# Kernel optimization log

Measured on AMD Instinct MI355X. Metric: run time of the kernel, lower is better.

The kernel has to match this reference:

```python
import jax, jax.numpy as jnp
import numpy as np

IN_CH = 128
INTER = max(IN_CH // 8, 1)  # 16

def setup_inputs() -> dict:
    key = jax.random.key(0)
    ks = jax.random.split(key, 10)
    B, C, D, H, W = 2, IN_CH, 16, 24, 24
    s = 1.0 / np.sqrt(C)
    so = 1.0 / np.sqrt(INTER)
    return {
        "x":  jax.random.normal(ks[0], (B, C, D, H, W), dtype=jnp.float32),
        "Wq": jax.random.normal(ks[1], (INTER, C), dtype=jnp.float32) * s,
        "bq": jax.random.normal(ks[2], (INTER,), dtype=jnp.float32) * 0.01,
        "Wk": jax.random.normal(ks[3], (INTER, C), dtype=jnp.float32) * s,
        "bk": jax.random.normal(ks[4], (INTER,), dtype=jnp.float32) * 0.01,
        "Wv": jax.random.normal(ks[5], (INTER, C), dtype=jnp.float32) * s,
        "bv": jax.random.normal(ks[6], (INTER,), dtype=jnp.float32) * 0.01,
        "Wo": jax.random.normal(ks[7], (C, INTER), dtype=jnp.float32) * so,
        "bo": jax.random.normal(ks[8], (C,), dtype=jnp.float32) * 0.01,
        "gamma": jnp.zeros((1,), dtype=jnp.float32) + 0.5,  # nonzero so attn path is exercised
    }

def reference(x, Wq, bq, Wk, bk, Wv, bv, Wo, bo, gamma):
    B, C, D, H, W = x.shape
    N = D * H * W
    xf = x.reshape(B, C, N)  # flatten spatial
    # 1x1x1 conv == per-voxel channel matmul
    q = jnp.einsum('ic,bcn->bin', Wq, xf) + bq[None, :, None]  # [B,I,N]
    k = jnp.einsum('ic,bcn->bin', Wk, xf) + bk[None, :, None]
    v = jnp.einsum('ic,bcn->bin', Wv, xf) + bv[None, :, None]
    # attention[b,n,m] = sum_i q[b,i,n] k[b,i,m]; softmax over keys m
    attn = jax.nn.softmax(jnp.einsum('bin,bim->bnm', q, k), axis=-1)
    # out[b,c,n] = sum_m v[b,c,m] attn[b,n,m]
    out = jnp.einsum('bim,bnm->bin', v, attn)  # [B,I,N]
    out = jnp.einsum('ci,bin->bcn', Wo, out) + bo[None, :, None]
    out = out.reshape(B, C, D, H, W)
    return gamma[0] * out + x
```

## Files before the change

kernel.cpp:

```cpp
#include <hip/hip_runtime.h>

#define C_CH 128
#define I_CH 16
#define NVOX 9216
#define BATCH 2
#define LOG2E 1.44269504088896340736f

typedef unsigned short ushort_t;
typedef unsigned int uint_t;
typedef short bf16x4 __attribute__((ext_vector_type(4)));
typedef short bf16x8 __attribute__((ext_vector_type(8)));
typedef float f32x4 __attribute__((ext_vector_type(4)));

static __device__ inline ushort_t f2bf_rne(float x) {
    uint_t u = __builtin_bit_cast(uint_t, x);
    u = (u + 0x7FFFu + ((u >> 16) & 1u)) >> 16;
    return (ushort_t)u;
}

static __device__ inline float fast_exp2(float x) {
#if __has_builtin(__builtin_amdgcn_exp2f)
    return __builtin_amdgcn_exp2f(x);
#else
    return exp2f(x);
#endif
}

static __device__ inline f32x4 score_mfma(bf16x4 a, bf16x4 b, f32x4 c) {
#if __has_builtin(__builtin_amdgcn_mfma_f32_16x16x16bf16_1k)
    return __builtin_amdgcn_mfma_f32_16x16x16bf16_1k(a, b, c, 0, 0, 0);
#elif __has_builtin(__builtin_amdgcn_mfma_f32_16x16x16_bf16)
    return __builtin_amdgcn_mfma_f32_16x16x16_bf16(a, b, c, 0, 0, 0);
#else
    int2 ai = __builtin_bit_cast(int2, a);
    int2 bi = __builtin_bit_cast(int2, b);
    int4 a4 = make_int4(ai.x, ai.y, 0, 0);
    int4 b4 = make_int4(bi.x, bi.y, 0, 0);
    return __builtin_amdgcn_mfma_f32_16x16x32_bf16(
        __builtin_bit_cast(bf16x8, a4), __builtin_bit_cast(bf16x8, b4), c, 0, 0, 0);
#endif
}

__global__ __launch_bounds__(256) void qkv_kernel(
    const float* __restrict__ x,
    const float* __restrict__ Wq, const float* __restrict__ bq,
    const float* __restrict__ Wk, const float* __restrict__ bk,
    const float* __restrict__ Wv, const float* __restrict__ bv,
    ushort_t* __restrict__ qb, ushort_t* __restrict__ kb,
    ushort_t* __restrict__ vT)
{
    __shared__ float ws[3][I_CH][132];
    __shared__ float xs[C_CH][I_CH];

    const int t    = threadIdx.x;
    const int vox0 = blockIdx.x * 16;
    const int b    = vox0 / NVOX;
    const int n0   = vox0 - b * NVOX;

    {
        const int i  = t >> 4;
        const int c8 = (t & 15) * 8;
        const float4* wq4 = (const float4*)(Wq + i * C_CH + c8);
        const float4* wk4 = (const float4*)(Wk + i * C_CH + c8);
        const float4* wv4 = (const float4*)(Wv + i * C_CH + c8);
        *(float4*)&ws[0][i][c8]     = wq4[0];
        *(float4*)&ws[0][i][c8 + 4] = wq4[1];
        *(float4*)&ws[1][i][c8]     = wk4[0];
        *(float4*)&ws[1][i][c8 + 4] = wk4[1];
        *(float4*)&ws[2][i][c8]     = wv4[0];
        *(float4*)&ws[2][i][c8 + 4] = wv4[1];
    }

    {
        const float* xb = x + (size_t)b * C_CH * NVOX + n0;
        const int c   = t >> 2;
        const int col = (t & 3) * 4;
        *(float4*)&xs[c][col]      = *(const float4*)(xb + (size_t)c * NVOX + col);
        *(float4*)&xs[c + 64][col] = *(const float4*)(xb + (size_t)(c + 64) * NVOX + col);
    }
    __syncthreads();

    const int n = t & 15;
    const int i = t >> 4;

    float aq = 0.f, ak = 0.f, av = 0.f;
    #pragma unroll 4
    for (int c = 0; c < C_CH; c += 4) {
        float x0 = xs[c + 0][n];
        float x1 = xs[c + 1][n];
        float x2 = xs[c + 2][n];
        float x3 = xs[c + 3][n];
        float4 wq = *(const float4*)&ws[0][i][c];
        float4 wk = *(const float4*)&ws[1][i][c];
        float4 wv = *(const float4*)&ws[2][i][c];
        aq = fmaf(wq.x, x0, fmaf(wq.y, x1, fmaf(wq.z, x2, fmaf(wq.w, x3, aq))));
        ak = fmaf(wk.x, x0, fmaf(wk.y, x1, fmaf(wk.z, x2, fmaf(wk.w, x3, ak))));
        av = fmaf(wv.x, x0, fmaf(wv.y, x1, fmaf(wv.z, x2, fmaf(wv.w, x3, av))));
    }

    const size_t vox = (size_t)vox0 + n;
    qb[vox * I_CH + i] = f2bf_rne((aq + bq[i]) * LOG2E);
    kb[vox * I_CH + i] = f2bf_rne(ak + bk[i]);
    vT[((size_t)b * I_CH + i) * NVOX + n0 + n] = f2bf_rne(av + bv[i]);
}

__global__ __launch_bounds__(512) void attn_kernel(
    const ushort_t* __restrict__ qb, const ushort_t* __restrict__ kb,
    const ushort_t* __restrict__ vT,
    const float* __restrict__ Wo, const float* __restrict__ bo,
    const float* __restrict__ gamma, const float* __restrict__ x,
    float* __restrict__ out)
{
    __shared__ float po[4][32][18];
    __shared__ float lsh[8][33];
    __shared__ float aot[16][40];
    __shared__ float wo_s[C_CH][17];

    const int tid  = threadIdx.x;
    const int w    = tid >> 6;
    const int lane = tid & 63;
    const int l16  = lane & 15;
    const int quad = lane >> 4;

    {
        const int c  = tid >> 2;
        const int i4 = (tid & 3) * 4;
        float4 wv = *(const float4*)(Wo + c * I_CH + i4);
        wo_s[c][i4 + 0] = wv.x; wo_s[c][i4 + 1] = wv.y;
        wo_s[c][i4 + 2] = wv.z; wo_s[c][i4 + 3] = wv.w;
    }

    const int qvox0 = blockIdx.x * 32;
    const int b     = qvox0 / NVOX;
    const int nloc0 = qvox0 - b * NVOX;

    bf16x4 qf0 = __builtin_bit_cast(bf16x4,
        *(const int2*)(qb + (size_t)(qvox0 + l16) * I_CH + quad * 4));
    bf16x4 qf1 = __builtin_bit_cast(bf16x4,
        *(const int2*)(qb + (size_t)(qvox0 + 16 + l16) * I_CH + quad * 4));

    const int p0     = ((l16 >> 2) << 3) + (l16 & 3);
    const int mchunk = w * (NVOX / 8);
    const ushort_t* kp = kb + ((size_t)b * NVOX + mchunk + p0) * I_CH + quad * 4;
    const ushort_t* vp = vT + ((size_t)b * I_CH + l16) * NVOX + mchunk + quad * 8;

    f32x4 O0 = {0.f,0.f,0.f,0.f}, O1 = {0.f,0.f,0.f,0.f};
    f32x4 L0 = {0.f,0.f,0.f,0.f}, L1 = {0.f,0.f,0.f,0.f};
    const f32x4 Z = {0.f,0.f,0.f,0.f};
    int4 onesi; onesi.x = onesi.y = onesi.z = onesi.w = 0x3F803F80;
    const bf16x8 ones = __builtin_bit_cast(bf16x8, onesi);

    int2 ka0 = *(const int2*)(kp);
    int2 ka1 = *(const int2*)(kp + 4 * I_CH);
    int4 va  = *(const int4*)(vp);

    #pragma unroll 2
    for (int it = 0; it < NVOX / 8 / 32; ++it) {
        kp += 32 * I_CH;
        vp += 32;
        int2 ka0n = *(const int2*)(kp);
        int2 ka1n = *(const int2*)(kp + 4 * I_CH);
        int4 van  = *(const int4*)(vp);

        bf16x4 kA0 = __builtin_bit_cast(bf16x4, ka0);
        bf16x4 kA1 = __builtin_bit_cast(bf16x4, ka1);
        f32x4 s00 = score_mfma(kA0, qf0, Z);
        f32x4 s01 = score_mfma(kA1, qf0, Z);
        f32x4 s10 = score_mfma(kA0, qf1, Z);
        f32x4 s11 = score_mfma(kA1, qf1, Z);

        {
            float p00 = fast_exp2(s00.x), p01 = fast_exp2(s00.y);
            float p02 = fast_exp2(s00.z), p03 = fast_exp2(s00.w);
            float p10 = fast_exp2(s01.x), p11 = fast_exp2(s01.y);
            float p12 = fast_exp2(s01.z), p13 = fast_exp2(s01.w);
            uint_t d0 = __builtin_amdgcn_perm(__builtin_bit_cast(uint_t, p01),
                                              __builtin_bit_cast(uint_t, p00), 0x07060302u);
            uint_t d1 = __builtin_amdgcn_perm(__builtin_bit_cast(uint_t, p03),
                                              __builtin_bit_cast(uint_t, p02), 0x07060302u);
            uint_t d2 = __builtin_amdgcn_perm(__builtin_bit_cast(uint_t, p11),
                                              __builtin_bit_cast(uint_t, p10), 0x07060302u);
            uint_t d3 = __builtin_amdgcn_perm(__builtin_bit_cast(uint_t, p13),
                                              __builtin_bit_cast(uint_t, p12), 0x07060302u);
            int4 pbi = make_int4((int)d0, (int)d1, (int)d2, (int)d3);
            bf16x8 pb = __builtin_bit_cast(bf16x8, pbi);
            O0 = __builtin_amdgcn_mfma_f32_16x16x32_bf16(
                __builtin_bit_cast(bf16x8, va), pb, O0, 0, 0, 0);
            L0 = __builtin_amdgcn_mfma_f32_16x16x32_bf16(ones, pb, L0, 0, 0, 0);
        }
        {
            float p00 = fast_exp2(s10.x), p01 = fast_exp2(s10.y);
            float p02 = fast_exp2(s10.z), p03 = fast_exp2(s10.w);
            float p10 = fast_exp2(s11.x), p11 = fast_exp2(s11.y);
            float p12 = fast_exp2(s11.z), p13 = fast_exp2(s11.w);
            uint_t d0 = __builtin_amdgcn_perm(__builtin_bit_cast(uint_t, p01),
                                              __builtin_bit_cast(uint_t, p00), 0x07060302u);
            uint_t d1 = __builtin_amdgcn_perm(__builtin_bit_cast(uint_t, p03),
                                              __builtin_bit_cast(uint_t, p02), 0x07060302u);
            uint_t d2 = __builtin_amdgcn_perm(__builtin_bit_cast(uint_t, p11),
                                              __builtin_bit_cast(uint_t, p10), 0x07060302u);
            uint_t d3 = __builtin_amdgcn_perm(__builtin_bit_cast(uint_t, p13),
                                              __builtin_bit_cast(uint_t, p12), 0x07060302u);
            int4 pbi = make_int4((int)d0, (int)d1, (int)d2, (int)d3);
            bf16x8 pb = __builtin_bit_cast(bf16x8, pbi);
            O1 = __builtin_amdgcn_mfma_f32_16x16x32_bf16(
                __builtin_bit_cast(bf16x8, va), pb, O1, 0, 0, 0);
            L1 = __builtin_amdgcn_mfma_f32_16x16x32_bf16(ones, pb, L1, 0, 0, 0);
        }

        ka0 = ka0n; ka1 = ka1n; va = van;
    }

    if (w < 4) {
        #pragma unroll
        for (int r = 0; r < 4; ++r) {
            po[w][quad * 4 + r][l16]      = O0[r];
            po[w][16 + quad * 4 + r][l16] = O1[r];
        }
    }
    if (quad == 0) { lsh[w][l16] = L0.x; lsh[w][16 + l16] = L1.x; }
    __syncthreads();

    if (w >= 4) {
        #pragma unroll
        for (int r = 0; r < 4; ++r) {
            po[w - 4][quad * 4 + r][l16]      += O0[r];
            po[w - 4][16 + quad * 4 + r][l16] += O1[r];
        }
    }
    __syncthreads();

    {
        const int q32 = tid & 31;
        const int i   = tid >> 5;
        const int row = (q32 >> 4) * 16 + i;
        const int col = q32 & 15;
        float v = 0.f, l = 0.f;
        #pragma unroll
        for (int ww = 0; ww < 4; ++ww) v += po[ww][row][col];
        #pragma unroll
        for (int ww = 0; ww < 8; ++ww) l += lsh[ww][q32];
        aot[i][q32] = v / l;
    }
    __syncthreads();

    const float g  = gamma[0];
    const int   c  = tid >> 2;
    const int   qh = (tid & 3) * 8;

    float acc[8];
    {
        const float b0 = bo[c];
        #pragma unroll
        for (int q = 0; q < 8; ++q) acc[q] = b0;
    }
    #pragma unroll
    for (int i = 0; i < 16; ++i) {
        const float wv = wo_s[c][i];
        float4 a0 = *(const float4*)&aot[i][qh];
        float4 a1 = *(const float4*)&aot[i][qh + 4];
        acc[0] = fmaf(wv, a0.x, acc[0]); acc[1] = fmaf(wv, a0.y, acc[1]);
        acc[2] = fmaf(wv, a0.z, acc[2]); acc[3] = fmaf(wv, a0.w, acc[3]);
        acc[4] = fmaf(wv, a1.x, acc[4]); acc[5] = fmaf(wv, a1.y, acc[5]);
        acc[6] = fmaf(wv, a1.z, acc[6]); acc[7] = fmaf(wv, a1.w, acc[7]);
    }

    const size_t gi = ((size_t)b * C_CH + c) * NVOX + nloc0 + qh;
    float4 x0 = *(const float4*)(x + gi);
    float4 x1 = *(const float4*)(x + gi + 4);
    float4 o0, o1;
    o0.x = fmaf(g, acc[0], x0.x); o0.y = fmaf(g, acc[1], x0.y);
    o0.z = fmaf(g, acc[2], x0.z); o0.w = fmaf(g, acc[3], x0.w);
    o1.x = fmaf(g, acc[4], x1.x); o1.y = fmaf(g, acc[5], x1.y);
    o1.z = fmaf(g, acc[6], x1.z); o1.w = fmaf(g, acc[7], x1.w);
    *(float4*)(out + gi)     = o0;
    *(float4*)(out + gi + 4) = o1;
}

extern "C" void kernel_launch(void* const* d_in, const int* in_sizes, int n_in,
                              void* d_out, int out_size, void* d_ws, size_t ws_size,
                              hipStream_t stream) {
    const float* x     = (const float*)d_in[0];
    const float* Wq    = (const float*)d_in[1];
    const float* bq    = (const float*)d_in[2];
    const float* Wk    = (const float*)d_in[3];
    const float* bk    = (const float*)d_in[4];
    const float* Wv    = (const float*)d_in[5];
    const float* bv    = (const float*)d_in[6];
    const float* Wo    = (const float*)d_in[7];
    const float* bo    = (const float*)d_in[8];
    const float* gamma = (const float*)d_in[9];
    float* out = (float*)d_out;

    ushort_t* qb = (ushort_t*)d_ws;
    ushort_t* kb = qb + (size_t)BATCH * NVOX * I_CH;
    ushort_t* vT = kb + (size_t)BATCH * NVOX * I_CH;

    hipLaunchKernelGGL(qkv_kernel, dim3(BATCH * NVOX / 16), dim3(256), 0, stream,
                       x, Wq, bq, Wk, bk, Wv, bv, qb, kb, vT);
    hipLaunchKernelGGL(attn_kernel, dim3(BATCH * NVOX / 32), dim3(512), 0, stream,
                       qb, kb, vT, Wo, bo, gamma, x, out);
}
```

Before: 127.9 us.

## Store K and V in MFMA fragment-ordered layout for contiguous per-lane loads

The QKV kernel now writes K and V in a pre-swizzled layout. Each 32-key group is laid out exactly as the attention kernel's MFMA lanes consume it, so every wave reads one contiguous 512-element block per iteration. Before, K was read with strided row gathers and V from a transposed array. This aims to make the attention inner-loop global loads fully coalesced and cheaper to address. In exchange the QKV kernel does scattered 2-byte stores with more index arithmetic.

```diff
diff --git a/kernel.cpp b/kernel.cpp
--- a/kernel.cpp
+++ b/kernel.cpp
@@ -4,6 +4,7 @@
 #define I_CH 16
 #define NVOX 9216
 #define BATCH 2
+#define NGRP (NVOX / 32)
 #define LOG2E 1.44269504088896340736f
 
 typedef unsigned short ushort_t;
@@ -46,8 +47,8 @@
     const float* __restrict__ Wq, const float* __restrict__ bq,
     const float* __restrict__ Wk, const float* __restrict__ bk,
     const float* __restrict__ Wv, const float* __restrict__ bv,
-    ushort_t* __restrict__ qb, ushort_t* __restrict__ kb,
-    ushort_t* __restrict__ vT)
+    ushort_t* __restrict__ qb, ushort_t* __restrict__ kfrag,
+    ushort_t* __restrict__ vfrag)
 {
     __shared__ float ws[3][I_CH][132];
     __shared__ float xs[C_CH][I_CH];
@@ -98,15 +99,30 @@
         av = fmaf(wv.x, x0, fmaf(wv.y, x1, fmaf(wv.z, x2, fmaf(wv.w, x3, av))));
     }
 
-    const size_t vox = (size_t)vox0 + n;
+    const int nl     = n0 + n;
+    const size_t vox = (size_t)b * NVOX + nl;
     qb[vox * I_CH + i] = f2bf_rne((aq + bq[i]) * LOG2E);
-    kb[vox * I_CH + i] = f2bf_rne(ak + bk[i]);
-    vT[((size_t)b * I_CH + i) * NVOX + n0 + n] = f2bf_rne(av + bv[i]);
+
+    const int g   = nl >> 5;
+    const int k32 = nl & 31;
+    const size_t gbase = ((size_t)b * NGRP + g) * 512;
+
+    {
+        const int tile = (k32 >> 2) & 1;
+        const int m    = k32 - 4 * tile;
+        const int l16  = ((m >> 3) << 2) | (m & 3);
+        const int lane = ((i >> 2) << 4) | l16;
+        kfrag[gbase + tile * 256 + lane * 4 + (i & 3)] = f2bf_rne(ak + bk[i]);
+    }
+    {
+        const int lane = ((k32 >> 3) << 4) | i;
+        vfrag[gbase + lane * 8 + (k32 & 7)] = f2bf_rne(av + bv[i]);
+    }
 }
 
 __global__ __launch_bounds__(512) void attn_kernel(
-    const ushort_t* __restrict__ qb, const ushort_t* __restrict__ kb,
-    const ushort_t* __restrict__ vT,
+    const ushort_t* __restrict__ qb, const ushort_t* __restrict__ kfrag,
+    const ushort_t* __restrict__ vfrag,
     const float* __restrict__ Wo, const float* __restrict__ bo,
     const float* __restrict__ gamma, const float* __restrict__ x,
     float* __restrict__ out)
@@ -139,10 +155,8 @@
     bf16x4 qf1 = __builtin_bit_cast(bf16x4,
         *(const int2*)(qb + (size_t)(qvox0 + 16 + l16) * I_CH + quad * 4));
 
-    const int p0     = ((l16 >> 2) << 3) + (l16 & 3);
-    const int mchunk = w * (NVOX / 8);
-    const ushort_t* kp = kb + ((size_t)b * NVOX + mchunk + p0) * I_CH + quad * 4;
-    const ushort_t* vp = vT + ((size_t)b * I_CH + l16) * NVOX + mchunk + quad * 8;
+    const ushort_t* kp = kfrag + ((size_t)b * NGRP + w * 36) * 512 + lane * 4;
+    const ushort_t* vp = vfrag + ((size_t)b * NGRP + w * 36) * 512 + lane * 8;
 
     f32x4 O0 = {0.f,0.f,0.f,0.f}, O1 = {0.f,0.f,0.f,0.f};
     f32x4 L0 = {0.f,0.f,0.f,0.f}, L1 = {0.f,0.f,0.f,0.f};
@@ -151,15 +165,15 @@
     const bf16x8 ones = __builtin_bit_cast(bf16x8, onesi);
 
     int2 ka0 = *(const int2*)(kp);
-    int2 ka1 = *(const int2*)(kp + 4 * I_CH);
+    int2 ka1 = *(const int2*)(kp + 256);
     int4 va  = *(const int4*)(vp);
 
     #pragma unroll 2
-    for (int it = 0; it < NVOX / 8 / 32; ++it) {
-        kp += 32 * I_CH;
-        vp += 32;
+    for (int it = 0; it < 36; ++it) {
+        kp += 512;
+        vp += 512;
         int2 ka0n = *(const int2*)(kp);
-        int2 ka1n = *(const int2*)(kp + 4 * I_CH);
+        int2 ka1n = *(const int2*)(kp + 256);
         int4 van  = *(const int4*)(vp);
 
         bf16x4 kA0 = __builtin_bit_cast(bf16x4, ka0);
@@ -292,12 +306,12 @@
     const float* gamma = (const float*)d_in[9];
     float* out = (float*)d_out;
 
-    ushort_t* qb = (ushort_t*)d_ws;
-    ushort_t* kb = qb + (size_t)BATCH * NVOX * I_CH;
-    ushort_t* vT = kb + (size_t)BATCH * NVOX * I_CH;
+    ushort_t* qb    = (ushort_t*)d_ws;
+    ushort_t* kfrag = qb    + (size_t)BATCH * NVOX * I_CH;
+    ushort_t* vfrag = kfrag + (size_t)BATCH * NGRP * 512;
 
     hipLaunchKernelGGL(qkv_kernel, dim3(BATCH * NVOX / 16), dim3(256), 0, stream,
-                       x, Wq, bq, Wk, bk, Wv, bv, qb, kb, vT);
+                       x, Wq, bq, Wk, bk, Wv, bv, qb, kfrag, vfrag);
     hipLaunchKernelGGL(attn_kernel, dim3(BATCH * NVOX / 32), dim3(512), 0, stream,
-                       qb, kb, vT, Wo, bo, gamma, x, out);
-}
+                       qb, kfrag, vfrag, Wo, bo, gamma, x, out);
+}
```

Measured after the change: 114.3 us, median of 2. -10.6%, faster.
